# Optimization experiments

Measured on AMD Instinct MI355X. Metric: run time of the kernel, lower is better.

## Reference

```python
import jax, jax.numpy as jnp
import numpy as np
from jax import lax

B, C_VIS, C_GRAPH, C_OUT, H, W, K = 8, 256, 256, 256, 96, 96, 3


def conv2d(x, w, b):
    # x: [B,Cin,H,W], w: [Cout,Cin,K,K], SAME padding (pad = K//2)
    y = lax.conv_general_dilated(x, w, window_strides=(1, 1), padding='SAME',
                                 dimension_numbers=('NCHW', 'OIHW', 'NCHW'))
    return y + b[None, :, None, None]


def setup_inputs() -> dict:
    key = jax.random.key(0)
    ks = jax.random.split(key, 12)
    scale_v = 1.0 / np.sqrt(C_VIS * K * K)
    scale_g = 1.0 / np.sqrt(C_GRAPH * K * K)
    scale_o = 1.0 / np.sqrt(C_OUT * K * K)
    return {
        'feats': jax.random.normal(ks[0], (B, C_VIS, H, W), jnp.float32),
        'graph_feature': jax.random.normal(ks[1], (B, C_GRAPH, H, W), jnp.float32),
        'wq': jax.random.normal(ks[2], (C_OUT, C_GRAPH, K, K), jnp.float32) * scale_g,
        'bq': jax.random.normal(ks[3], (C_OUT,), jnp.float32) * 0.01,
        'wk': jax.random.normal(ks[4], (C_OUT, C_VIS, K, K), jnp.float32) * scale_v,
        'bk': jax.random.normal(ks[5], (C_OUT,), jnp.float32) * 0.01,
        'wv': jax.random.normal(ks[6], (C_OUT, C_VIS, K, K), jnp.float32) * scale_v,
        'bv': jax.random.normal(ks[7], (C_OUT,), jnp.float32) * 0.01,
        'wo': jax.random.normal(ks[8], (C_OUT, C_OUT, K, K), jnp.float32) * scale_o,
        'bo': jax.random.normal(ks[9], (C_OUT,), jnp.float32) * 0.01,
    }


def reference(feats, graph_feature, wq, bq, wk, bk, wv, bv, wo, bo):
    q = conv2d(graph_feature, wq, bq)  # [B,C,H,W]
    k = conv2d(feats, wk, bk)          # [B,C,H,W]
    v = conv2d(feats, wv, bv)          # [B,C,H,W]
    # attention over rows: attn[b,c,i,j] = sum_w q[b,c,i,w] * k[b,c,j,w]
    scale = 1.0 / jnp.sqrt(jnp.asarray(k.shape[-1], q.dtype))
    attn = jnp.einsum('bchw,bcgw->bchg', q, k) * scale  # [B,C,H,H]
    attn = jax.nn.softmax(attn, axis=-1)
    fused = jnp.einsum('bchg,bcgw->bchw', attn, v)      # [B,C,H,W]
    return conv2d(fused, wo, bo)
```

## Files before the change

### kernel.cpp

```cpp
#include <hip/hip_runtime.h>
#include <hip/hip_bf16.h>

constexpr int BATCH = 8;
constexpr int CH    = 256;
constexpr int H     = 96;
constexpr int W     = 96;
constexpr int HW    = H * W;
constexpr long PLANE_ELEMS = (long)BATCH * CH * HW;
constexpr int PAD   = 98;

typedef short  bf16x8_t __attribute__((ext_vector_type(8)));
typedef float  f32x4_t  __attribute__((ext_vector_type(4)));

__device__ inline uint pk2_bf16(float a, float b) {
  ushort lo = __bfloat16_as_ushort(__float2bfloat16(a));
  ushort hi = __bfloat16_as_ushort(__float2bfloat16(b));
  return (uint)lo | ((uint)hi << 16);
}

#define WAITVM(N) asm volatile("s_waitcnt vmcnt(" #N ")" ::: "memory")

__device__ __forceinline__ void gl_lds16(const ushort* g, ushort* l) {
  __builtin_amdgcn_global_load_lds(
      (const __attribute__((address_space(1))) void*)g,
      (__attribute__((address_space(3))) void*)l, 16, 0, 0);
}

__global__ __launch_bounds__(256) void prep_wb(
    const float* __restrict__ s0, const float* __restrict__ s1,
    const float* __restrict__ s2, const float* __restrict__ s3,
    ushort* __restrict__ d0, ushort* __restrict__ d1,
    ushort* __restrict__ d2, ushort* __restrict__ d3,
    ushort* __restrict__ p0, ushort* __restrict__ p1)
{
  if (blockIdx.x < 9216) {
    const int t = blockIdx.x / 2304;
    const int idx = (blockIdx.x % 2304) * 256 + threadIdx.x;
    const float* s = (t == 0) ? s0 : (t == 1) ? s1 : (t == 2) ? s2 : s3;
    ushort* d      = (t == 0) ? d0 : (t == 1) ? d1 : (t == 2) ? d2 : d3;
    const int e   = idx & 7;
    const int lg  = (idx >> 3) & 3;
    const int l15 = (idx >> 5) & 15;
    const int q   = (idx >> 9) & 15;
    const int cc  = (idx >> 13) & 7;
    const int tap = idx >> 16;
    const int co  = q * 16 + l15;
    const int ci  = cc * 32 + lg * 8 + e;
    d[idx] = __bfloat16_as_ushort(__float2bfloat16(s[(co * 256 + ci) * 9 + tap]));
    return;
  }
  const int bb = blockIdx.x - 9216;
  const int ub = bb % 49;
  const int b  = (bb / 49) & 7;
  ushort* p = (bb >= 392) ? p1 : p0;
  const int u = ub * 256 + threadIdx.x;
  if (u >= 12416) return;
  int y, x, cu;
  if (u < 6272)      { y = (u < 3136) ? 0 : 97; int r = u % 3136; x = r >> 5; cu = r & 31; }
  else               { int r = u - 6272; x = (r < 3072) ? 0 : 97; int r2 = r % 3072; y = 1 + (r2 >> 5); cu = r2 & 31; }
  int4 z = make_int4(0, 0, 0, 0);
  *(int4*)&p[(((long)b * PAD + y) * PAD + x) * 256 + cu * 8] = z;
}

__global__ __launch_bounds__(256) void nchw_f32_to_nhwc_bf16_2(
    const float* __restrict__ in0, const float* __restrict__ in1,
    ushort* __restrict__ out0, ushort* __restrict__ out1)
{
  __shared__ float t[32][33];
  const int tid = threadIdx.x;
  const int p0 = blockIdx.x * 32;
  const int c0 = blockIdx.y * 32;
  const int ts = blockIdx.z >> 3;
  const int b  = blockIdx.z & 7;
  const float* in = ts ? in1 : in0;
  ushort* out     = ts ? out1 : out0;
  const int tp = tid & 31, tc8 = tid >> 5;
#pragma unroll
  for (int i = 0; i < 4; ++i) {
    int c = tc8 + i * 8;
    t[c][tp] = in[((long)(b * 256 + c0 + c)) * HW + p0 + tp];
  }
  __syncthreads();
  const int wc = tid & 31, wp8 = tid >> 5;
#pragma unroll
  for (int i = 0; i < 4; ++i) {
    int p = p0 + wp8 + i * 8;
    int y = p / 96, x = p % 96;
    out[(((long)b * PAD + y + 1) * PAD + x + 1) * 256 + c0 + wc] =
        __bfloat16_as_ushort(__float2bfloat16(t[wc][wp8 + i * 8]));
  }
}

__global__ __launch_bounds__(256) void nchw_bf16_to_nhwc_bf16(
    const ushort* __restrict__ in, ushort* __restrict__ out)
{
  __shared__ ushort t[32][34];
  const int tid = threadIdx.x;
  const int p0 = blockIdx.x * 32;
  const int c0 = blockIdx.y * 32;
  const int b  = blockIdx.z;
  const int tp = tid & 31, tc8 = tid >> 5;
#pragma unroll
  for (int i = 0; i < 4; ++i) {
    int c = tc8 + i * 8;
    t[c][tp] = in[((long)(b * 256 + c0 + c)) * HW + p0 + tp];
  }
  __syncthreads();
  const int wc = tid & 31, wp8 = tid >> 5;
#pragma unroll
  for (int i = 0; i < 4; ++i) {
    int p = p0 + wp8 + i * 8;
    int y = p / 96, x = p % 96;
    out[(((long)b * PAD + y + 1) * PAD + x + 1) * 256 + c0 + wc] = t[wc][wp8 + i * 8];
  }
}

template <int NT, typename OutT>
__global__ __launch_bounds__(256, 2) void conv3x3_mfma(
    const ushort* pin0, const ushort* pin1,
    const ushort* w0, const ushort* w1, const ushort* w2,
    const float* bias0, const float* bias1, const float* bias2,
    OutT* o0, OutT* o1, OutT* o2)
{
  const int tid  = threadIdx.x;
  const int lane = tid & 63;
  const int wv   = tid >> 6;
  const int wm   = wv & 1;
  const int wn   = wv >> 1;
  const int l15  = lane & 15;
  const int lg   = lane >> 4;

  const int nwg = NT * 768;
  const int cpx = nwg >> 3;
  const int swz = ((int)blockIdx.x & 7) * cpx + ((int)blockIdx.x >> 3);
  const int t    = swz / 768;
  const int rest = swz % 768;
  const ushort* pin = (t == 2) ? pin1 : pin0;
  const ushort* wt  = (t == 0) ? w0 : (t == 1) ? w1 : w2;
  const float* bias = (t == 0) ? bias0 : (t == 1) ? bias1 : bias2;
  OutT* out         = (t == 0) ? o0 : (t == 1) ? o1 : o2;

  const int cox = rest & 1;
  const int yb  = (rest >> 1) % 48;
  const int b   = (rest >> 1) / 48;
  const int co0 = cox * 128;
  const int y0  = yb * 2;
  const int coq = cox * 8 + wm * 4;
  const int alo = (l15 * 4 + lg) << 3;

  __shared__ ushort sIn[2][1568 * 8];

  f32x4_t acc[4][6];
#pragma unroll
  for (int m = 0; m < 4; ++m)
#pragma unroll
    for (int n = 0; n < 6; ++n)
      acc[m][n] = (f32x4_t){0.f, 0.f, 0.f, 0.f};

  auto issueIN = [&](int cc) {
    const int ci0 = cc * 32;
    const int ubase = wv * 392;
#pragma unroll
    for (int it = 0; it < 7; ++it) {
      int lo = it * 64 + lane;
      if (lo < 392) {
        int u  = ubase + lo;
        int q  = u >> 2;
        int g  = u & 3;
        int xx = q % 98, rr = q / 98;
        int ug = g ^ ((xx + (xx >> 2)) & 3);
        const ushort* src = pin + (((long)(b * PAD + y0 + rr)) * PAD + xx) * 256 + ci0 + ug * 8;
        ushort* dst = (ushort*)((char*)&sIn[cc & 1][0] + (long)u * 16);
        gl_lds16(src, dst);
      }
    }
  };

  auto glda = [&](int tap, int cc, int m) -> bf16x8_t {
    return *(const bf16x8_t*)&wt[(((tap * 8 + cc) * 16 + coq + m) << 9) + alo];
  };

  bf16x8_t a0[4], a1[4], a2[4];

#define ISSUE_A(CC, TAP, AR)                \
  if ((CC) < 8) {                           \
    AR[0] = glda((TAP), (CC), 0);           \
    AR[1] = glda((TAP), (CC), 1);           \
    AR[2] = glda((TAP), (CC), 2);           \
    AR[3] = glda((TAP), (CC), 3);           \
  }

  auto dotap = [&](int DY, int DX, int bi, const bf16x8_t* a) {
    bf16x8_t bb[6];
    const char* Bb = (const char*)&sIn[bi][0];
    const int s    = l15 + DX;
    const int boff = (lg ^ ((s + (s >> 2)) & 3)) << 4;
    const int rr   = wn + DY;
#pragma unroll
    for (int n = 0; n < 6; ++n)
      bb[n] = *(const bf16x8_t*)(Bb + ((rr * 98 + n * 16 + s) << 6) + boff);
    __builtin_amdgcn_s_setprio(1);
#pragma unroll
    for (int m = 0; m < 4; ++m)
#pragma unroll
      for (int n = 0; n < 6; ++n)
        acc[m][n] = __builtin_amdgcn_mfma_f32_16x16x32_bf16(
            a[m], bb[n], acc[m][n], 0, 0, 0);
    __builtin_amdgcn_s_setprio(0);
  };

  issueIN(0);
  __builtin_amdgcn_sched_barrier(0);
  ISSUE_A(0, 0, a0);
  ISSUE_A(0, 1, a1);
  __builtin_amdgcn_sched_barrier(0);
  WAITVM(8);
  __builtin_amdgcn_s_barrier();
  __builtin_amdgcn_sched_barrier(0);

#pragma unroll 1
  for (int c = 0; c < 8; ++c) {
    const int bi = c & 1;
    if (c < 7) issueIN(c + 1);
    __builtin_amdgcn_sched_barrier(0);
    ISSUE_A(c, 2, a2)  dotap(0, 0, bi, a0);
    ISSUE_A(c, 3, a0)  dotap(0, 1, bi, a1);
    ISSUE_A(c, 4, a1)  dotap(0, 2, bi, a2);
    ISSUE_A(c, 5, a2)  dotap(1, 0, bi, a0);
    ISSUE_A(c, 6, a0)  dotap(1, 1, bi, a1);
    ISSUE_A(c, 7, a1)  dotap(1, 2, bi, a2);
    ISSUE_A(c, 8, a2)  dotap(2, 0, bi, a0);
    ISSUE_A(c + 1, 0, a0)  dotap(2, 1, bi, a1);
    ISSUE_A(c + 1, 1, a1)  dotap(2, 2, bi, a2);
    __builtin_amdgcn_sched_barrier(0);
    if (c < 7) { WAITVM(36); } else { WAITVM(0); }
    __builtin_amdgcn_s_barrier();
    __builtin_amdgcn_sched_barrier(0);
  }
#undef ISSUE_A

  if constexpr (sizeof(OutT) == 2) {
    char* sE = (char*)&sIn[0][0];
#pragma unroll
    for (int h = 0; h < 2; ++h) {
      if (wm == h) {
#pragma unroll
        for (int m = 0; m < 4; ++m)
#pragma unroll
          for (int r = 0; r < 4; ++r) {
            const int col = m * 16 + lg * 4 + r;
            const float bv = bias[co0 + h * 64 + col];
#pragma unroll
            for (int n = 0; n < 6; ++n) {
              *(ushort*)(sE + col * 400 + (wn * 96 + n * 16 + l15) * 2) =
                  __bfloat16_as_ushort(__float2bfloat16(acc[m][n][r] + bv));
            }
          }
      }
      __syncthreads();
#pragma unroll
      for (int it = 0; it < 7; ++it) {
        int u = it * 256 + tid;
        if (u < 1600) {
          int co = u / 25, ru = u % 25;
          if (ru < 24) {
            int4 v = *(const int4*)(sE + co * 400 + ru * 16);
            int e0 = ru * 8;
            int yy = y0 + (e0 >= 96);
            int x  = e0 - (e0 >= 96 ? 96 : 0);
            *(int4*)&out[(((long)(b * 256 + co0 + h * 64 + co)) * 96 + yy) * 96 + x] = v;
          }
        }
      }
      __syncthreads();
    }
  } else {
    char* sE = (char*)&sIn[0][0];
#pragma unroll
    for (int h = 0; h < 2; ++h) {
      if (wm == h) {
#pragma unroll
        for (int m = 0; m < 4; ++m)
#pragma unroll
          for (int r = 0; r < 4; ++r) {
            const int col = m * 16 + lg * 4 + r;
            const float bv = bias[co0 + h * 64 + col];
#pragma unroll
            for (int n = 0; n < 6; ++n) {
              *(float*)(sE + (col * 196 + wn * 96 + n * 16 + l15) * 4) =
                  acc[m][n][r] + bv;
            }
          }
      }
      __syncthreads();
#pragma unroll
      for (int it = 0; it < 12; ++it) {
        int u = it * 256 + tid;
        int co = u / 48, ru = u % 48;
        int4 v = *(const int4*)(sE + (co * 196 + ru * 4) * 4);
        int e0 = ru * 4;
        int yy = y0 + (e0 >= 96);
        int x  = e0 - (e0 >= 96 ? 96 : 0);
        *(int4*)&out[(((long)(b * 256 + co0 + h * 64 + co)) * 96 + yy) * 96 + x] = v;
      }
      __syncthreads();
    }
  }
}

constexpr int APITCH = 104;

__global__ __launch_bounds__(384, 3) void attn_mfma(
    const ushort* __restrict__ q,
    const ushort* __restrict__ k,
    const ushort* __restrict__ v,
    ushort* __restrict__ outf)
{
  __shared__ ushort sK [96 * APITCH];
  __shared__ ushort sVt[96 * APITCH];
  __shared__ ushort sP [6 * 16 * APITCH];

  const int tid  = threadIdx.x;
  const int lane = tid & 63;
  const int wv   = tid >> 6;
  const int l15  = lane & 15;
  const int lg   = lane >> 4;
  const long plane = (long)blockIdx.x * HW;

  for (int u = tid; u < 1152; u += 384) {
    int j = u / 12, c8 = u % 12;
    *(int4*)&sK[j * APITCH + c8 * 8] = *(const int4*)&k[plane + j * 96 + c8 * 8];
  }
  for (int u = tid; u < 1152; u += 384) {
    int j = u % 96, c8 = u / 96;
    ushort tmp[8];
    *(int4*)tmp = *(const int4*)&v[plane + j * 96 + c8 * 8];
#pragma unroll
    for (int e = 0; e < 8; ++e)
      sVt[(c8 * 8 + e) * APITCH + j] = tmp[e];
  }
  __syncthreads();

  const int i0 = wv * 16;

  bf16x8_t qf[3];
#pragma unroll
  for (int ks = 0; ks < 3; ++ks)
    qf[ks] = *(const bf16x8_t*)&q[plane + (i0 + l15) * 96 + ks * 32 + lg * 8];

  f32x4_t s[6];
#pragma unroll
  for (int jt = 0; jt < 6; ++jt) s[jt] = (f32x4_t){0.f, 0.f, 0.f, 0.f};
#pragma unroll
  for (int jt = 0; jt < 6; ++jt)
#pragma unroll
    for (int ks = 0; ks < 3; ++ks) {
      bf16x8_t kf = *(const bf16x8_t*)&sK[(jt * 16 + l15) * APITCH + ks * 32 + lg * 8];
      s[jt] = __builtin_amdgcn_mfma_f32_16x16x32_bf16(kf, qf[ks], s[jt], 0, 0, 0);
    }

  const float sc = 0.10206207261596575f;
  float m = -3.0e38f;
#pragma unroll
  for (int jt = 0; jt < 6; ++jt)
#pragma unroll
    for (int r = 0; r < 4; ++r) m = fmaxf(m, s[jt][r]);
  m = fmaxf(m, __shfl_xor(m, 16));
  m = fmaxf(m, __shfl_xor(m, 32));

  float p[6][4];
  float sum = 0.f;
#pragma unroll
  for (int jt = 0; jt < 6; ++jt)
#pragma unroll
    for (int r = 0; r < 4; ++r) {
      float e = __expf((s[jt][r] - m) * sc);
      p[jt][r] = e;
      sum += e;
    }
  sum += __shfl_xor(sum, 16);
  sum += __shfl_xor(sum, 32);
  const float inv = 1.f / sum;

  ushort* myP = &sP[wv * 16 * APITCH];
#pragma unroll
  for (int jt = 0; jt < 6; ++jt) {
    *(uint*)&myP[l15 * APITCH + jt * 16 + lg * 4] =
        pk2_bf16(p[jt][0] * inv, p[jt][1] * inv);
    *(uint*)&myP[l15 * APITCH + jt * 16 + lg * 4 + 2] =
        pk2_bf16(p[jt][2] * inv, p[jt][3] * inv);
  }

  bf16x8_t pf[3];
#pragma unroll
  for (int ks = 0; ks < 3; ++ks)
    pf[ks] = *(const bf16x8_t*)&myP[l15 * APITCH + ks * 32 + lg * 8];

  f32x4_t o[6];
#pragma unroll
  for (int wt = 0; wt < 6; ++wt) o[wt] = (f32x4_t){0.f, 0.f, 0.f, 0.f};
#pragma unroll
  for (int wt = 0; wt < 6; ++wt)
#pragma unroll
    for (int ks = 0; ks < 3; ++ks) {
      bf16x8_t vf = *(const bf16x8_t*)&sVt[(wt * 16 + l15) * APITCH + ks * 32 + lg * 8];
      o[wt] = __builtin_amdgcn_mfma_f32_16x16x32_bf16(pf[ks], vf, o[wt], 0, 0, 0);
    }

#pragma unroll
  for (int wt = 0; wt < 6; ++wt)
#pragma unroll
    for (int r = 0; r < 4; ++r) {
      int i = i0 + lg * 4 + r;
      outf[plane + i * 96 + wt * 16 + l15] =
          __bfloat16_as_ushort(__float2bfloat16(o[wt][r]));
    }
}

extern "C" void kernel_launch(void* const* d_in, const int* in_sizes, int n_in,
                              void* d_out, int out_size, void* d_ws, size_t ws_size,
                              hipStream_t stream) {
  (void)in_sizes; (void)n_in; (void)out_size; (void)ws_size;

  const float* feats = (const float*)d_in[0];
  const float* graph = (const float*)d_in[1];
  const float* wq    = (const float*)d_in[2];
  const float* bq    = (const float*)d_in[3];
  const float* wk    = (const float*)d_in[4];
  const float* bk    = (const float*)d_in[5];
  const float* wv    = (const float*)d_in[6];
  const float* bv    = (const float*)d_in[7];
  const float* wo    = (const float*)d_in[8];
  const float* bo    = (const float*)d_in[9];
  float* out = (float*)d_out;

  char* ws = (char*)d_ws;
  const long planeB   = PLANE_ELEMS * 2;
  const long pinElems = (long)BATCH * PAD * PAD * 256;
  ushort* qb   = (ushort*)ws;
  ushort* kb   = (ushort*)(ws + planeB);
  ushort* vb   = (ushort*)(ws + 2 * planeB);
  ushort* pinF = (ushort*)(ws + 3 * planeB);
  ushort* pinG = pinF + pinElems;
  ushort* wtq  = pinG + pinElems;
  ushort* wtk  = wtq + 9 * 256 * 256;
  ushort* wtv  = wtk + 9 * 256 * 256;
  ushort* wto  = wtv + 9 * 256 * 256;

  dim3 tgrid2(HW / 32, CH / 32, 2 * BATCH);
  dim3 tgrid (HW / 32, CH / 32, BATCH);
  dim3 agrid (BATCH * CH);

  prep_wb<<<9216 + 784, 256, 0, stream>>>(wq, wk, wv, wo, wtq, wtk, wtv, wto,
                                          pinF, pinG);

  nchw_f32_to_nhwc_bf16_2<<<tgrid2, 256, 0, stream>>>(feats, graph, pinF, pinG);

  conv3x3_mfma<3, ushort><<<3 * 768, 256, 0, stream>>>(
      pinF, pinG, wtk, wtv, wtq, bk, bv, bq, kb, vb, qb);

  attn_mfma<<<agrid, 384, 0, stream>>>(qb, kb, vb, qb);

  nchw_bf16_to_nhwc_bf16<<<tgrid, 256, 0, stream>>>(qb, pinF);

  conv3x3_mfma<1, float><<<768, 256, 0, stream>>>(
      pinF, pinF, wto, wto, wto, bo, bo, bo, out, out, out);
}
```

Baseline: 397.3 us.

## Switch conv MFMA from 16x16x32 to 32x32x16 bf16 tiles

Rewrites the implicit-GEMM 3x3 conv inner loop to use 32x32x16 bf16 MFMA instructions instead of 16x16x32, and changes the weight pre-pack layout, the LDS operand fetch pattern and the epilogue accumulator-to-column mapping to match. Larger MFMA tiles need fewer B-operand LDS reads per FLOP and fewer instructions. The trade-off is a different LDS bank access pattern under the existing swizzle and accumulators held as 16-wide vectors, which may change register pressure.

```diff
diff --git a/kernel.cpp b/kernel.cpp
--- a/kernel.cpp
+++ b/kernel.cpp
@@ -9,8 +9,9 @@
 constexpr long PLANE_ELEMS = (long)BATCH * CH * HW;
 constexpr int PAD   = 98;
 
-typedef short  bf16x8_t __attribute__((ext_vector_type(8)));
-typedef float  f32x4_t  __attribute__((ext_vector_type(4)));
+typedef short  bf16x8_t  __attribute__((ext_vector_type(8)));
+typedef float  f32x4_t   __attribute__((ext_vector_type(4)));
+typedef float  f32x16_t  __attribute__((ext_vector_type(16)));
 
 __device__ inline uint pk2_bf16(float a, float b) {
   ushort lo = __bfloat16_as_ushort(__float2bfloat16(a));
@@ -38,14 +39,14 @@
     const int idx = (blockIdx.x % 2304) * 256 + threadIdx.x;
     const float* s = (t == 0) ? s0 : (t == 1) ? s1 : (t == 2) ? s2 : s3;
     ushort* d      = (t == 0) ? d0 : (t == 1) ? d1 : (t == 2) ? d2 : d3;
-    const int e   = idx & 7;
-    const int lg  = (idx >> 3) & 3;
-    const int l15 = (idx >> 5) & 15;
-    const int q   = (idx >> 9) & 15;
-    const int cc  = (idx >> 13) & 7;
-    const int tap = idx >> 16;
-    const int co  = q * 16 + l15;
-    const int ci  = cc * 32 + lg * 8 + e;
+    const int e    = idx & 7;
+    const int lane = (idx >> 3) & 63;
+    const int kh   = (idx >> 9) & 1;
+    const int q32  = (idx >> 10) & 7;
+    const int cc   = (idx >> 13) & 7;
+    const int tap  = idx >> 16;
+    const int co   = q32 * 32 + (lane & 31);
+    const int ci   = cc * 32 + kh * 16 + (lane >> 5) * 8 + e;
     d[idx] = __bfloat16_as_ushort(__float2bfloat16(s[(co * 256 + ci) * 9 + tap]));
     return;
   }
@@ -127,8 +128,8 @@
   const int wv   = tid >> 6;
   const int wm   = wv & 1;
   const int wn   = wv >> 1;
-  const int l15  = lane & 15;
-  const int lg   = lane >> 4;
+  const int l31  = lane & 31;
+  const int hi   = lane >> 5;
 
   const int nwg = NT * 768;
   const int cpx = nwg >> 3;
@@ -145,17 +146,17 @@
   const int b   = (rest >> 1) / 48;
   const int co0 = cox * 128;
   const int y0  = yb * 2;
-  const int coq = cox * 8 + wm * 4;
-  const int alo = (l15 * 4 + lg) << 3;
+  const int q32b = cox * 4 + wm * 2;
 
   __shared__ ushort sIn[2][1568 * 8];
 
-  f32x4_t acc[4][6];
-#pragma unroll
-  for (int m = 0; m < 4; ++m)
-#pragma unroll
-    for (int n = 0; n < 6; ++n)
-      acc[m][n] = (f32x4_t){0.f, 0.f, 0.f, 0.f};
+  f32x16_t acc[2][3];
+#pragma unroll
+  for (int ct = 0; ct < 2; ++ct)
+#pragma unroll
+    for (int pt = 0; pt < 3; ++pt)
+#pragma unroll
+      for (int e = 0; e < 16; ++e) acc[ct][pt][e] = 0.f;
 
   auto issueIN = [&](int cc) {
     const int ci0 = cc * 32;
@@ -176,8 +177,9 @@
     }
   };
 
-  auto glda = [&](int tap, int cc, int m) -> bf16x8_t {
-    return *(const bf16x8_t*)&wt[(((tap * 8 + cc) * 16 + coq + m) << 9) + alo];
+  auto glda = [&](int tap, int cc, int f) -> bf16x8_t {
+    return *(const bf16x8_t*)&wt[((((tap * 8 + cc) * 8 + q32b + (f >> 1)) * 2
+                                   + (f & 1)) << 9) + (lane << 3)];
   };
 
   bf16x8_t a0[4], a1[4], a2[4];
@@ -193,19 +195,26 @@
   auto dotap = [&](int DY, int DX, int bi, const bf16x8_t* a) {
     bf16x8_t bb[6];
     const char* Bb = (const char*)&sIn[bi][0];
-    const int s    = l15 + DX;
-    const int boff = (lg ^ ((s + (s >> 2)) & 3)) << 4;
     const int rr   = wn + DY;
 #pragma unroll
-    for (int n = 0; n < 6; ++n)
-      bb[n] = *(const bf16x8_t*)(Bb + ((rr * 98 + n * 16 + s) << 6) + boff);
+    for (int pt = 0; pt < 3; ++pt) {
+      const int s = pt * 32 + l31 + DX;
+      const int sw = (s + (s >> 2)) & 3;
+#pragma unroll
+      for (int kh = 0; kh < 2; ++kh) {
+        const int g = ((kh << 1) | hi) ^ sw;
+        bb[pt * 2 + kh] = *(const bf16x8_t*)(Bb + ((rr * 98 + s) << 6) + (g << 4));
+      }
+    }
     __builtin_amdgcn_s_setprio(1);
 #pragma unroll
-    for (int m = 0; m < 4; ++m)
-#pragma unroll
-      for (int n = 0; n < 6; ++n)
-        acc[m][n] = __builtin_amdgcn_mfma_f32_16x16x32_bf16(
-            a[m], bb[n], acc[m][n], 0, 0, 0);
+    for (int kh = 0; kh < 2; ++kh)
+#pragma unroll
+      for (int ct = 0; ct < 2; ++ct)
+#pragma unroll
+        for (int pt = 0; pt < 3; ++pt)
+          acc[ct][pt] = __builtin_amdgcn_mfma_f32_32x32x16_bf16(
+              a[ct * 2 + kh], bb[pt * 2 + kh], acc[ct][pt], 0, 0, 0);
     __builtin_amdgcn_s_setprio(0);
   };
 
@@ -245,15 +254,15 @@
     for (int h = 0; h < 2; ++h) {
       if (wm == h) {
 #pragma unroll
-        for (int m = 0; m < 4; ++m)
-#pragma unroll
-          for (int r = 0; r < 4; ++r) {
-            const int col = m * 16 + lg * 4 + r;
+        for (int ct = 0; ct < 2; ++ct)
+#pragma unroll
+          for (int r = 0; r < 16; ++r) {
+            const int col = ct * 32 + (r & 3) + 8 * (r >> 2) + 4 * hi;
             const float bv = bias[co0 + h * 64 + col];
 #pragma unroll
-            for (int n = 0; n < 6; ++n) {
-              *(ushort*)(sE + col * 400 + (wn * 96 + n * 16 + l15) * 2) =
-                  __bfloat16_as_ushort(__float2bfloat16(acc[m][n][r] + bv));
+            for (int pt = 0; pt < 3; ++pt) {
+              *(ushort*)(sE + col * 400 + (wn * 96 + pt * 32 + l31) * 2) =
+                  __bfloat16_as_ushort(__float2bfloat16(acc[ct][pt][r] + bv));
             }
           }
       }
@@ -280,15 +289,15 @@
     for (int h = 0; h < 2; ++h) {
       if (wm == h) {
 #pragma unroll
-        for (int m = 0; m < 4; ++m)
-#pragma unroll
-          for (int r = 0; r < 4; ++r) {
-            const int col = m * 16 + lg * 4 + r;
+        for (int ct = 0; ct < 2; ++ct)
+#pragma unroll
+          for (int r = 0; r < 16; ++r) {
+            const int col = ct * 32 + (r & 3) + 8 * (r >> 2) + 4 * hi;
             const float bv = bias[co0 + h * 64 + col];
 #pragma unroll
-            for (int n = 0; n < 6; ++n) {
-              *(float*)(sE + (col * 196 + wn * 96 + n * 16 + l15) * 4) =
-                  acc[m][n][r] + bv;
+            for (int pt = 0; pt < 3; ++pt) {
+              *(float*)(sE + (col * 196 + wn * 96 + pt * 32 + l31) * 4) =
+                  acc[ct][pt][r] + bv;
             }
           }
       }
```

Result: slower. 416.9 us (+4.9%).
